# Kernel optimization log

Hardware: AMD Instinct MI355X
Metric: run time of the kernel (lower is better)

Reference implementation:

```python
import jax, jax.numpy as jnp
import numpy as np


def setup_inputs() -> dict:
    key = jax.random.key(0)
    k1, k2, k3, k4 = jax.random.split(key, 4)
    B, T, E, D = 4, 4096, 2048, 128
    x = jax.random.normal(k1, (B, T, E), dtype=jnp.float32)
    # nn.Linear(E, D, bias=False): y = x @ W where W is [E, D]
    scale = 1.0 / np.sqrt(E)
    Wq = jax.random.normal(k2, (E, D), dtype=jnp.float32) * scale
    Wk = jax.random.normal(k3, (E, D), dtype=jnp.float32) * scale
    Wv = jax.random.normal(k4, (E, D), dtype=jnp.float32) * scale
    return {"x": x, "Wq": Wq, "Wk": Wk, "Wv": Wv}


def reference(x, Wq, Wk, Wv):
    # Single attention head, prefill path (kv_cache=None, T_q == T_k).
    D = Wq.shape[1]
    Q = jnp.einsum('bte,ed->btd', x, Wq)
    K = jnp.einsum('bte,ed->btd', x, Wk)
    V = jnp.einsum('bte,ed->btd', x, Wv)
    scores = jnp.einsum('bqd,bkd->bqk', Q, K) / jnp.sqrt(jnp.float32(D))
    T = x.shape[1]
    causal = jnp.tril(jnp.ones((T, T), dtype=bool))  # [T_q, T_k]
    scores = jnp.where(causal[None, :, :], scores, -jnp.inf)
    attn = jax.nn.softmax(scores, axis=-1)
    out = jnp.einsum('bqk,bkd->bqd', attn, V)
    return out
```

## Files before the change

kernel.cpp:

```cpp
#include <hip/hip_runtime.h>
#include <hip/hip_bf16.h>

typedef short bf16x8 __attribute__((ext_vector_type(8)));
typedef float f32x4  __attribute__((ext_vector_type(4)));

#define T_SEQ 4096
#define NB    4
#define E_DIM 2048
#define D_DIM 128
#define M_TOT (NB * T_SEQ)
#define NCHUNK 4
#define CHUNK_KT 16
#define SM_SHIFT 12.0f

__device__ __forceinline__ ushort f2bf(float f) {
  union { float f; unsigned u; } c; c.f = f;
  unsigned u = c.u;
  unsigned r = (u + 0x7FFFu + ((u >> 16) & 1u)) >> 16;
  return (ushort)r;
}
__device__ __forceinline__ float bf2f(ushort u) {
  union { unsigned u; float f; } c; c.u = ((unsigned)u) << 16;
  return c.f;
}
__device__ __forceinline__ bf16x8 cvt8(const float4& lo, const float4& hi) {
  union { __hip_bfloat162 h; ushort u[2]; } t;
  union { ushort u[8]; bf16x8 v; } r;
  t.h = __float22bfloat162_rn(make_float2(lo.x, lo.y)); r.u[0] = t.u[0]; r.u[1] = t.u[1];
  t.h = __float22bfloat162_rn(make_float2(lo.z, lo.w)); r.u[2] = t.u[0]; r.u[3] = t.u[1];
  t.h = __float22bfloat162_rn(make_float2(hi.x, hi.y)); r.u[4] = t.u[0]; r.u[5] = t.u[1];
  t.h = __float22bfloat162_rn(make_float2(hi.z, hi.w)); r.u[6] = t.u[0]; r.u[7] = t.u[1];
  return r.v;
}

__device__ __forceinline__ void gl2lds16(const void* g, void* l) {
  __builtin_amdgcn_global_load_lds(
      (const __attribute__((address_space(1))) unsigned int*)g,
      (__attribute__((address_space(3))) unsigned int*)l, 16, 0, 0);
}

__global__ __launch_bounds__(256) void build_wt(const float* __restrict__ Wq,
                                                const float* __restrict__ Wk,
                                                const float* __restrict__ Wv,
                                                ushort* __restrict__ Wt) {
  __shared__ ushort tile[64][72];
  const int tid = threadIdx.x;
  const int k0 = blockIdx.x * 64, n0 = blockIdx.y * 64, o = blockIdx.z;
  const float* W = (o == 0) ? Wq : ((o == 1) ? Wk : Wv);
  for (int i = 0; i < 4; i++) {
    int c = tid + i * 256;
    int r = c >> 4, c4 = (c & 15) * 4;
    float4 v = *(const float4*)(W + (size_t)(k0 + r) * D_DIM + n0 + c4);
    ushort4 b4;
    b4.x = f2bf(v.x); b4.y = f2bf(v.y); b4.z = f2bf(v.z); b4.w = f2bf(v.w);
    *(ushort4*)(&tile[r][c4]) = b4;
  }
  __syncthreads();
  for (int i = 0; i < 2; i++) {
    int c = tid + i * 256;
    int nn = c >> 3, k8 = (c & 7) * 8;
    ushort tmp[8];
    for (int j = 0; j < 8; j++) tmp[j] = tile[k8 + j][nn];
    *(uint4*)(Wt + (size_t)((o << 7) + n0 + nn) * E_DIM + k0 + k8) = *(const uint4*)tmp;
  }
}

__global__ __launch_bounds__(256, 4) void qkv_gemm(const float* __restrict__ x,
                                                   const ushort* __restrict__ Wt,
                                                   ushort* __restrict__ Q,
                                                   ushort* __restrict__ K,
                                                   ushort* __restrict__ Vt) {
  __shared__ ushort As[2][64 * 64];
  __shared__ ushort Bs[2][96 * 64];

  const int tid  = threadIdx.x;
  const int wave = tid >> 6, lane = tid & 63;
  const int quad = lane >> 4, l16 = lane & 15;
  const int wm = wave >> 1, wn = wave & 1;
  const int m0 = blockIdx.x * 64;
  const int n0 = blockIdx.y * 96;

  f32x4 acc[2][3] = {};

  const int s_ = wave * 64 + lane;
  const int n_ = s_ >> 3, p_ = s_ & 7;

  const int ar_ = tid >> 2, aq4_ = tid & 3;
  const float* xrow = x + (size_t)(m0 + ar_) * E_DIM + aq4_ * 16;

#define DMA_B(k0_, buf_)                                                        \
  _Pragma("unroll")                                                             \
  for (int i_ = 0; i_ < 3; i_++) {                                              \
    int slotbase = i_ * 256 + wave * 64;                                        \
    int n = (i_ * 32) + n_;                           \
    int cg = p_ ^ (n & 7);                                                      \
    gl2lds16(Wt + (size_t)(n0 + n) * E_DIM + (k0_) + cg * 8,                    \
             (char*)(buf_) + (size_t)slotbase * 16);                            \
  }

#define GLOAD_A(k0_)                                                            \
  {                                                                             \
    const float* ap_ = xrow + (k0_);                                            \
    areg0 = *(const float4*)(ap_);                                              \
    areg1 = *(const float4*)(ap_ + 4);                                          \
    areg2 = *(const float4*)(ap_ + 8);                                          \
    areg3 = *(const float4*)(ap_ + 12);                                         \
  }

#define CVT_WRITE_A(bufidx)                                                     \
  {                                                                             \
    ushort* as_ = As[bufidx];                                                   \
    bf16x8 w0_ = cvt8(areg0, areg1);                                            \
    bf16x8 w1_ = cvt8(areg2, areg3);                                            \
    *(bf16x8*)(as_ + ar_ * 64 + (((aq4_ * 2)     ^ (ar_ & 7)) * 8)) = w0_;      \
    *(bf16x8*)(as_ + ar_ * 64 + (((aq4_ * 2 + 1) ^ (ar_ & 7)) * 8)) = w1_;      \
  }

#define COMPUTE(bufidx)                                                         \
  {                                                                             \
    const ushort* as_ = As[bufidx];                                             \
    const ushort* bs_ = Bs[bufidx];                                             \
    _Pragma("unroll")                                                           \
    for (int kk = 0; kk < 2; kk++) {                                            \
      const int slot = ((kk * 4 + quad) ^ (l16 & 7)) * 8;                       \
      bf16x8 af0 = *(const bf16x8*)(as_ + (wm * 32 + l16) * 64 + slot);         \
      bf16x8 af1 = *(const bf16x8*)(as_ + (wm * 32 + 16 + l16) * 64 + slot);    \
      _Pragma("unroll")                                                         \
      for (int ni = 0; ni < 3; ni++) {                                          \
        int n = wn * 48 + ni * 16 + l16;                                        \
        bf16x8 bf = *(const bf16x8*)(bs_ + n * 64 + slot);                      \
        acc[0][ni] = __builtin_amdgcn_mfma_f32_16x16x32_bf16(af0, bf, acc[0][ni], 0, 0, 0); \
        acc[1][ni] = __builtin_amdgcn_mfma_f32_16x16x32_bf16(af1, bf, acc[1][ni], 0, 0, 0); \
      }                                                                         \
    }                                                                           \
  }

  float4 areg0, areg1, areg2, areg3;

  GLOAD_A(0);
  DMA_B(0, Bs[0]);
  CVT_WRITE_A(0);
  __syncthreads();

  for (int it = 0; it < 32; it += 2) {
    GLOAD_A((it + 1) * 64);
    DMA_B((it + 1) * 64, Bs[1]);
    COMPUTE(0);
    CVT_WRITE_A(1);
    __syncthreads();
    if (it < 30) {
      GLOAD_A((it + 2) * 64);
      DMA_B((it + 2) * 64, Bs[0]);
      COMPUTE(1);
      CVT_WRITE_A(0);
      __syncthreads();
    } else {
      COMPUTE(1);
    }
  }

  const int b  = m0 >> 12;
  const int t0 = m0 & 4095;
  const int dbase2 = (n0 == 192) ? 0 : 32;
  ushort* vtile = (ushort*)As;

  __syncthreads();

  for (int mi = 0; mi < 2; mi++)
    for (int ni = 0; ni < 3; ni++) {
      int colall = n0 + wn * 48 + ni * 16 + l16;
      int o = colall >> 7, d = colall & 127;
      if (o < 2) {
        ushort* dst = o ? K : Q;
        for (int r = 0; r < 4; r++) {
          int row = m0 + wm * 32 + mi * 16 + quad * 4 + r;
          dst[(size_t)row * D_DIM + d] = f2bf(acc[mi][ni][r]);
        }
      } else {
        int dloc = d - dbase2;
        for (int r = 0; r < 4; r++) {
          int mloc = wm * 32 + mi * 16 + quad * 4 + r;
          vtile[dloc * 72 + mloc] = f2bf(acc[mi][ni][r]);
        }
      }
    }

  if (n0 >= 192) {
    __syncthreads();
    const int nrows = (n0 == 192) ? 32 : 96;
    if (tid < nrows * 2) {
      int dloc = tid >> 1, half = tid & 1;
      const ushort* src = vtile + dloc * 72 + half * 32;
      ushort* dstp = Vt + (size_t)(b * D_DIM + dbase2 + dloc) * T_SEQ + t0 + half * 32;
#pragma unroll
      for (int j = 0; j < 4; j++)
        ((uint4*)dstp)[j] = ((const uint4*)src)[j];
    }
  }
#undef DMA_B
#undef GLOAD_A
#undef CVT_WRITE_A
#undef COMPUTE
}

__global__ __launch_bounds__(256) void attn_partial(const ushort* __restrict__ Q,
                                                    const ushort* __restrict__ K,
                                                    const ushort* __restrict__ Vt,
                                                    ushort* __restrict__ Po,
                                                    float* __restrict__ Ll) {
  const int qt = blockIdx.x, cq = blockIdx.y, b = blockIdx.z;
  const int kt0 = cq * CHUNK_KT;
  if (kt0 > qt) return;

  __shared__ ushort Kt[64][136];
  __shared__ ushort Vts[128][72];
  __shared__ ushort Pls[4][16][72];

  const int tid = threadIdx.x;
  const int wave = tid >> 6, lane = tid & 63;
  const int quad = lane >> 4, l16 = lane & 15;

  const int qrow = qt * 64 + wave * 16 + l16;
  bf16x8 qf[4];
  for (int kk = 0; kk < 4; kk++)
    qf[kk] = *(const bf16x8*)(Q + (size_t)(b * T_SEQ + qrow) * D_DIM + kk * 32 + quad * 8);

  bf16x8 ones;
  for (int j = 0; j < 8; j++) ones[j] = (short)0x3F80;

  f32x4 o_acc[8] = {};
  f32x4 lacc = {};
  const float scale2 = 0.08838834764831845f * 1.4426950408889634f;

  const int kt1 = min(qt, kt0 + CHUNK_KT - 1);

  for (int kt = kt0; kt <= kt1; kt++) {
    __syncthreads();
    for (int i = 0; i < 4; i++) {
      int c = tid + i * 256;
      int r = c >> 4, col = (c & 15) * 8;
      *(uint4*)(&Kt[r][col]) = *(const uint4*)(K + (size_t)(b * T_SEQ + kt * 64 + r) * D_DIM + col);
    }
    for (int i = 0; i < 4; i++) {
      int c = tid + i * 256;
      int dr = c >> 3, col = (c & 7) * 8;
      *(uint4*)(&Vts[dr][col]) = *(const uint4*)(Vt + (size_t)(b * D_DIM + dr) * T_SEQ + kt * 64 + col);
    }
    __syncthreads();

    f32x4 s[4] = {};
    for (int kk = 0; kk < 4; kk++) {
      const int kc = kk * 32 + quad * 8;
      for (int ni = 0; ni < 4; ni++) {
        bf16x8 bf = *(const bf16x8*)(&Kt[ni * 16 + l16][kc]);
        s[ni] = __builtin_amdgcn_mfma_f32_16x16x32_bf16(qf[kk], bf, s[ni], 0, 0, 0);
      }
    }
    if (kt == qt) {
      for (int ni = 0; ni < 4; ni++) {
        int kidx = kt * 64 + ni * 16 + l16;
        for (int r = 0; r < 4; r++) {
          int qidx = qt * 64 + wave * 16 + quad * 4 + r;
          float v = (kidx > qidx) ? -1e30f : (s[ni][r] * scale2 - SM_SHIFT);
          s[ni][r] = exp2f(v);
        }
      }
    } else {
      for (int ni = 0; ni < 4; ni++)
        for (int r = 0; r < 4; r++)
          s[ni][r] = exp2f(s[ni][r] * scale2 - SM_SHIFT);
    }
    for (int ni = 0; ni < 4; ni++)
      for (int r = 0; r < 4; r++)
        Pls[wave][quad * 4 + r][ni * 16 + l16] = f2bf(s[ni][r]);
    for (int kk2 = 0; kk2 < 2; kk2++) {
      const int kc = kk2 * 32 + quad * 8;
      bf16x8 pf = *(const bf16x8*)(&Pls[wave][l16][kc]);
      for (int ni = 0; ni < 8; ni++) {
        bf16x8 vf = *(const bf16x8*)(&Vts[ni * 16 + l16][kc]);
        o_acc[ni] = __builtin_amdgcn_mfma_f32_16x16x32_bf16(pf, vf, o_acc[ni], 0, 0, 0);
      }
      lacc = __builtin_amdgcn_mfma_f32_16x16x32_bf16(pf, ones, lacc, 0, 0, 0);
    }
  }

  const int slot = (b * 64 + qt) * NCHUNK + cq;
  for (int ni = 0; ni < 8; ni++)
    for (int r = 0; r < 4; r++) {
      int ql = wave * 16 + quad * 4 + r;
      Po[(size_t)slot * 8192 + ql * D_DIM + ni * 16 + l16] = f2bf(o_acc[ni][r]);
    }
  if (l16 == 0) {
    for (int r = 0; r < 4; r++) {
      int ql = wave * 16 + quad * 4 + r;
      Ll[slot * 64 + ql] = lacc[r];
    }
  }
}

__global__ __launch_bounds__(256) void attn_reduce(const ushort* __restrict__ Po,
                                                   const float* __restrict__ Ll,
                                                   float* __restrict__ out) {
  const int qt = blockIdx.x, b = blockIdx.y;
  const int nc = qt / CHUNK_KT + 1;
  const int tid = threadIdx.x;
  const int row = tid >> 2;
  const int c0  = (tid & 3) * 32;
  const int base_slot = (b * 64 + qt) * NCHUNK;

  float L = 0.f;
  for (int c = 0; c < nc; c++) L += Ll[(base_slot + c) * 64 + row];
  const float inv = 1.0f / L;

  const size_t orow = (size_t)(b * T_SEQ + qt * 64 + row) * D_DIM;
  for (int cc = 0; cc < 32; cc += 8) {
    float a[8] = {0,0,0,0,0,0,0,0};
    for (int c = 0; c < nc; c++) {
      const ushort* p = Po + (size_t)(base_slot + c) * 8192 + row * D_DIM + c0 + cc;
      ushort u[8];
      *(uint4*)u = *(const uint4*)p;
      for (int j = 0; j < 8; j++) a[j] += bf2f(u[j]);
    }
    float4 o0, o1;
    o0.x = a[0] * inv; o0.y = a[1] * inv; o0.z = a[2] * inv; o0.w = a[3] * inv;
    o1.x = a[4] * inv; o1.y = a[5] * inv; o1.z = a[6] * inv; o1.w = a[7] * inv;
    *(float4*)(out + orow + c0 + cc)     = o0;
    *(float4*)(out + orow + c0 + cc + 4) = o1;
  }
}

extern "C" void kernel_launch(void* const* d_in, const int* in_sizes, int n_in,
                              void* d_out, int out_size, void* d_ws, size_t ws_size,
                              hipStream_t stream) {
  const float* x  = (const float*)d_in[0];
  const float* Wq = (const float*)d_in[1];
  const float* Wk = (const float*)d_in[2];
  const float* Wv = (const float*)d_in[3];
  float* out = (float*)d_out;

  ushort* Q  = (ushort*)d_ws;
  ushort* Kb = Q  + (size_t)M_TOT * D_DIM;
  ushort* Vb = Kb + (size_t)M_TOT * D_DIM;
  ushort* Vt = Vb + (size_t)M_TOT * D_DIM;
  ushort* Wt = Vt + (size_t)M_TOT * D_DIM;
  ushort* Po = Wt + (size_t)384 * E_DIM;
  float*  Ll = (float*)(Po + (size_t)NB * 64 * NCHUNK * 8192);

  hipLaunchKernelGGL(build_wt,     dim3(32, 2, 3),       dim3(256), 0, stream, Wq, Wk, Wv, Wt);
  hipLaunchKernelGGL(qkv_gemm,     dim3(256, 4),         dim3(256), 0, stream, x, Wt, Q, Kb, Vt);
  hipLaunchKernelGGL(attn_partial, dim3(64, NCHUNK, 4),  dim3(256), 0, stream, Q, Kb, Vt, Po, Ll);
  hipLaunchKernelGGL(attn_reduce,  dim3(64, 4),          dim3(256), 0, stream, Po, Ll, out);
}
```

Before: 295.1 us.

## Load K and V fragments directly from global memory instead of LDS staging

Drops the shared-memory staging of K and V tiles and the two block barriers per key tile. Each wave now reads its MFMA operand fragments straight from global memory, relying on L1/L2 to absorb the reuse across the four waves. Loops are also explicitly unrolled. This removes the barrier and LDS round-trip, but it issues four times the global load traffic per tile and exposes load latency directly in front of the MFMAs.

```diff
diff --git a/kernel.cpp b/kernel.cpp
--- a/kernel.cpp
+++ b/kernel.cpp
@@ -212,8 +212,6 @@
   const int kt0 = cq * CHUNK_KT;
   if (kt0 > qt) return;
 
-  __shared__ ushort Kt[64][136];
-  __shared__ ushort Vts[128][72];
   __shared__ ushort Pls[4][16][72];
 
   const int tid = threadIdx.x;
@@ -222,10 +220,12 @@
 
   const int qrow = qt * 64 + wave * 16 + l16;
   bf16x8 qf[4];
+#pragma unroll
   for (int kk = 0; kk < 4; kk++)
     qf[kk] = *(const bf16x8*)(Q + (size_t)(b * T_SEQ + qrow) * D_DIM + kk * 32 + quad * 8);
 
   bf16x8 ones;
+#pragma unroll
   for (int j = 0; j < 8; j++) ones[j] = (short)0x3F80;
 
   f32x4 o_acc[8] = {};
@@ -234,31 +234,25 @@
 
   const int kt1 = min(qt, kt0 + CHUNK_KT - 1);
 
+  const ushort* Kb  = K  + (size_t)b * T_SEQ * D_DIM;
+  const ushort* Vtb = Vt + (size_t)b * D_DIM * T_SEQ;
+
   for (int kt = kt0; kt <= kt1; kt++) {
-    __syncthreads();
-    for (int i = 0; i < 4; i++) {
-      int c = tid + i * 256;
-      int r = c >> 4, col = (c & 15) * 8;
-      *(uint4*)(&Kt[r][col]) = *(const uint4*)(K + (size_t)(b * T_SEQ + kt * 64 + r) * D_DIM + col);
-    }
-    for (int i = 0; i < 4; i++) {
-      int c = tid + i * 256;
-      int dr = c >> 3, col = (c & 7) * 8;
-      *(uint4*)(&Vts[dr][col]) = *(const uint4*)(Vt + (size_t)(b * D_DIM + dr) * T_SEQ + kt * 64 + col);
-    }
-    __syncthreads();
-
     f32x4 s[4] = {};
+#pragma unroll
     for (int kk = 0; kk < 4; kk++) {
       const int kc = kk * 32 + quad * 8;
+#pragma unroll
       for (int ni = 0; ni < 4; ni++) {
-        bf16x8 bf = *(const bf16x8*)(&Kt[ni * 16 + l16][kc]);
+        bf16x8 bf = *(const bf16x8*)(Kb + (size_t)(kt * 64 + ni * 16 + l16) * D_DIM + kc);
         s[ni] = __builtin_amdgcn_mfma_f32_16x16x32_bf16(qf[kk], bf, s[ni], 0, 0, 0);
       }
     }
     if (kt == qt) {
+#pragma unroll
       for (int ni = 0; ni < 4; ni++) {
         int kidx = kt * 64 + ni * 16 + l16;
+#pragma unroll
         for (int r = 0; r < 4; r++) {
           int qidx = qt * 64 + wave * 16 + quad * 4 + r;
           float v = (kidx > qidx) ? -1e30f : (s[ni][r] * scale2 - SM_SHIFT);
@@ -266,18 +260,24 @@
         }
       }
     } else {
+#pragma unroll
       for (int ni = 0; ni < 4; ni++)
+#pragma unroll
         for (int r = 0; r < 4; r++)
           s[ni][r] = exp2f(s[ni][r] * scale2 - SM_SHIFT);
     }
+#pragma unroll
     for (int ni = 0; ni < 4; ni++)
+#pragma unroll
       for (int r = 0; r < 4; r++)
         Pls[wave][quad * 4 + r][ni * 16 + l16] = f2bf(s[ni][r]);
+#pragma unroll
     for (int kk2 = 0; kk2 < 2; kk2++) {
       const int kc = kk2 * 32 + quad * 8;
       bf16x8 pf = *(const bf16x8*)(&Pls[wave][l16][kc]);
+#pragma unroll
       for (int ni = 0; ni < 8; ni++) {
-        bf16x8 vf = *(const bf16x8*)(&Vts[ni * 16 + l16][kc]);
+        bf16x8 vf = *(const bf16x8*)(Vtb + (size_t)(ni * 16 + l16) * T_SEQ + kt * 64 + kc);
         o_acc[ni] = __builtin_amdgcn_mfma_f32_16x16x32_bf16(pf, vf, o_acc[ni], 0, 0, 0);
       }
       lacc = __builtin_amdgcn_mfma_f32_16x16x32_bf16(pf, ones, lacc, 0, 0, 0);
@@ -285,12 +285,15 @@
   }
 
   const int slot = (b * 64 + qt) * NCHUNK + cq;
+#pragma unroll
   for (int ni = 0; ni < 8; ni++)
+#pragma unroll
     for (int r = 0; r < 4; r++) {
       int ql = wave * 16 + quad * 4 + r;
       Po[(size_t)slot * 8192 + ql * D_DIM + ni * 16 + l16] = f2bf(o_acc[ni][r]);
     }
   if (l16 == 0) {
+#pragma unroll
     for (int r = 0; r < 4; r++) {
       int ql = wave * 16 + quad * 4 + r;
       Ll[slot * 64 + ql] = lacc[r];
```

New measurement: 416.4 us. 1.41x slower.
